# Performance work log

Measured on AMD Instinct MI355X. Metric: run time of the kernel, lower is better.

Reference implementation:

```python
import jax, jax.numpy as jnp
import numpy as np

N, E, NFEAT, NHID, NCLASS = 50000, 800000, 256, 128, 16
NTRAIN, NTEST, K = 5000, 5000, 20


def setup_inputs() -> dict:
    key = jax.random.key(0)
    ks = jax.random.split(key, 10)
    features = jax.random.normal(ks[0], (N, NFEAT), dtype=jnp.float32)
    edge_index = jax.random.randint(ks[1], (2, E), 0, N, dtype=jnp.int64)
    edge_weight = jax.random.uniform(ks[2], (E,), dtype=jnp.float32)
    labels = jax.random.randint(ks[3], (N,), 0, NCLASS)
    onehot_labels = jax.nn.one_hot(labels, NCLASS, dtype=jnp.float32)
    idx_train = jax.random.randint(ks[4], (NTRAIN,), 0, N, dtype=jnp.int64)
    idx_test = jax.random.randint(ks[5], (NTEST,), 0, N, dtype=jnp.int64)
    # GCN parameters (2-layer: nfeat->nhid->nhid), glorot-ish init
    W1 = jax.random.normal(ks[6], (NFEAT, NHID), dtype=jnp.float32) / np.sqrt(NFEAT)
    b1 = jnp.zeros((NHID,), dtype=jnp.float32)
    W2 = jax.random.normal(ks[7], (NHID, NHID), dtype=jnp.float32) / np.sqrt(NHID)
    b2 = jnp.zeros((NHID,), dtype=jnp.float32)
    return {"features": features, "edge_weight": edge_weight,
            "onehot_labels": onehot_labels, "W1": W1, "b1": b1,
            "W2": W2, "b2": b2, "edge_index": edge_index,
            "idx_train": idx_train, "idx_test": idx_test}


def _propagate(h, edge_index, edge_weight, n_nodes):
    # out[dst] += w * h[src]  (weighted message passing)
    src, dst = edge_index[0], edge_index[1]
    return jax.ops.segment_sum(h[src] * edge_weight[:, None], dst,
                               num_segments=n_nodes)


def reference(features, edge_weight, onehot_labels, W1, b1, W2, b2,
              edge_index, idx_train, idx_test):
    n_nodes = features.shape[0]
    # 2-layer GCN: transform then propagate (efficient order)
    h = _propagate(features @ W1, edge_index, edge_weight, n_nodes) + b1
    h = jax.nn.relu(h)
    emb = _propagate(h @ W2, edge_index, edge_weight, n_nodes) + b2

    # KNN scoring: [n_test, n_train] similarity matrix
    score = emb[idx_test] @ emb[idx_train].T
    # keep top-K largest per row (original masks the n_train-K smallest with -inf)
    vals, idx = jax.lax.top_k(score, K)
    rows = jnp.arange(score.shape[0])[:, None]
    masked = jnp.full_like(score, -jnp.inf).at[rows, idx].set(vals)
    weights = jax.nn.softmax(masked, axis=1)
    preds = weights @ onehot_labels[idx_train]
    return preds
```

## Files before the change

kernel.cpp:

```cpp
#include <hip/hip_runtime.h>
#include <math.h>
#include <limits.h>

#define NNODE 50000
#define NEDGE 800000
#define NFEAT 256
#define NHID  128
#define NTEST 5000
#define NTRAIN 5000
#define NCLS  16
#define TOPK  20
#define CB    640
#define NCT   8
#define RB    32
#define NTPAD (NCT * CB)
#define CCAP  512

typedef __attribute__((ext_vector_type(8))) short short8v;
typedef __attribute__((ext_vector_type(4))) short short4v;
typedef __attribute__((ext_vector_type(4))) float f32x4;

__device__ inline int swz(int r, int c) {
  int cc = c + 4 * r;
  cc = (cc < CB) ? cc : cc - CB;
  return r * CB + cc;
}

__device__ inline void splitbf(float x, unsigned short& h, unsigned short& l) {
  unsigned u = __float_as_uint(x);
  unsigned hb = (u + 0x7fffu + ((u >> 16) & 1u)) >> 16;
  float hf = __uint_as_float(hb << 16);
  float r = x - hf;
  unsigned ur = __float_as_uint(r);
  unsigned lb = (ur + 0x7fffu + ((ur >> 16) & 1u)) >> 16;
  h = (unsigned short)hb; l = (unsigned short)lb;
}

__device__ inline void split8(float4 a0, float4 a1, short8v& h, short8v& l) {
  unsigned short hh, ll;
  splitbf(a0.x, hh, ll); h[0] = (short)hh; l[0] = (short)ll;
  splitbf(a0.y, hh, ll); h[1] = (short)hh; l[1] = (short)ll;
  splitbf(a0.z, hh, ll); h[2] = (short)hh; l[2] = (short)ll;
  splitbf(a0.w, hh, ll); h[3] = (short)hh; l[3] = (short)ll;
  splitbf(a1.x, hh, ll); h[4] = (short)hh; l[4] = (short)ll;
  splitbf(a1.y, hh, ll); h[5] = (short)hh; l[5] = (short)ll;
  splitbf(a1.z, hh, ll); h[6] = (short)hh; l[6] = (short)ll;
  splitbf(a1.w, hh, ll); h[7] = (short)hh; l[7] = (short)ll;
}

__global__ __launch_bounds__(256)
void prep0(int* __restrict__ cursor,
           const float* __restrict__ W1, unsigned short* __restrict__ WT1hi,
           unsigned short* __restrict__ WT1lo,
           const float* __restrict__ W2, unsigned short* __restrict__ WT2hi,
           unsigned short* __restrict__ WT2lo,
           const float* __restrict__ onehot, const int* __restrict__ itr,
           float* __restrict__ lab, int* __restrict__ ccnt) {
  int gid = blockIdx.x * 256 + threadIdx.x;
  if (gid < NNODE) {
    cursor[gid] = 0;
  } else if (gid < NNODE + NFEAT * 128) {
    int i = gid - NNODE;
    int n = i / NFEAT, k = i - n * NFEAT;
    unsigned short h, l;
    splitbf(W1[(size_t)k * 128 + n], h, l);
    WT1hi[i] = h; WT1lo[i] = l;
  } else if (gid < NNODE + NFEAT * 128 + NHID * 128) {
    int i = gid - NNODE - NFEAT * 128;
    int n = i / NHID, k = i - n * NHID;
    unsigned short h, l;
    splitbf(W2[(size_t)k * 128 + n], h, l);
    WT2hi[i] = h; WT2lo[i] = l;
  } else if (gid < NNODE + NFEAT * 128 + NHID * 128 + NTRAIN * NCLS) {
    int i = gid - NNODE - NFEAT * 128 - NHID * 128;
    int j = i >> 4, c = i & 15;
    lab[i] = onehot[(size_t)itr[j] * NCLS + c];
  } else if (gid < NNODE + NFEAT * 128 + NHID * 128 + NTRAIN * NCLS + NTEST) {
    ccnt[gid - NNODE - NFEAT * 128 - NHID * 128 - NTRAIN * NCLS] = 0;
  }
}

template<int KT, bool RELU>
__global__ __launch_bounds__(256)
void gemm_mfma(const float* __restrict__ A, const unsigned short* __restrict__ WThi,
               const unsigned short* __restrict__ WTlo, float* __restrict__ C, int M) {
  const int tid = threadIdx.x;
  const int w = tid >> 6, lane = tid & 63;
  const int m0 = blockIdx.x * 64 + w * 16;
  int arow = m0 + (lane & 15); if (arow > M - 1) arow = M - 1;
  const int koff = (lane >> 4) * 8;

  f32x4 acc[8];
#pragma unroll
  for (int t = 0; t < 8; ++t) acc[t] = {0.f, 0.f, 0.f, 0.f};

#pragma unroll
  for (int ks = 0; ks < KT / 32; ++ks) {
    const float* ap = &A[(size_t)arow * KT + ks * 32 + koff];
    float4 a0 = *reinterpret_cast<const float4*>(ap);
    float4 a1 = *reinterpret_cast<const float4*>(ap + 4);
    if (RELU) {
      a0.x=fmaxf(a0.x,0.f); a0.y=fmaxf(a0.y,0.f); a0.z=fmaxf(a0.z,0.f); a0.w=fmaxf(a0.w,0.f);
      a1.x=fmaxf(a1.x,0.f); a1.y=fmaxf(a1.y,0.f); a1.z=fmaxf(a1.z,0.f); a1.w=fmaxf(a1.w,0.f);
    }
    short8v ah, al;
    split8(a0, a1, ah, al);
#pragma unroll
    for (int t = 0; t < 8; ++t) {
      size_t bo = (size_t)(t * 16 + (lane & 15)) * KT + ks * 32 + koff;
      short8v bh = *reinterpret_cast<const short8v*>(&WThi[bo]);
      short8v bl = *reinterpret_cast<const short8v*>(&WTlo[bo]);
      acc[t] = __builtin_amdgcn_mfma_f32_16x16x32_bf16(ah, bh, acc[t], 0, 0, 0);
      acc[t] = __builtin_amdgcn_mfma_f32_16x16x32_bf16(ah, bl, acc[t], 0, 0, 0);
      acc[t] = __builtin_amdgcn_mfma_f32_16x16x32_bf16(al, bh, acc[t], 0, 0, 0);
    }
  }
  const int crow0 = m0 + (lane >> 4) * 4;
#pragma unroll
  for (int j = 0; j < 4; ++j) {
    int row = crow0 + j;
    if (row < M) {
#pragma unroll
      for (int t = 0; t < 8; ++t)
        C[(size_t)row * 128 + t * 16 + (lane & 15)] = acc[t][j];
    }
  }
}

__global__ __launch_bounds__(256)
void hist_dst(const int* __restrict__ edst, int* __restrict__ cnt) {
  int e = blockIdx.x * 256 + threadIdx.x;
  if (e < NEDGE) atomicAdd(&cnt[edst[e]], 1);
}

#define SCHUNK 196
__global__ __launch_bounds__(256)
void scan_cnt(int* __restrict__ cnt) {
  __shared__ int part[256];
  const int t = threadIdx.x;
  const int base = t * SCHUNK;
  int s = 0;
  for (int i = 0; i < SCHUNK / 4; ++i) {
    int idx = base + i * 4;
    if (idx + 3 < NNODE) {
      int4 v = *reinterpret_cast<const int4*>(&cnt[idx]);
      s += v.x + v.y + v.z + v.w;
    } else {
      for (int j = 0; j < 4; ++j) if (idx + j < NNODE) s += cnt[idx + j];
    }
  }
  part[t] = s;
  __syncthreads();
  for (int off = 1; off < 256; off <<= 1) {
    int v = (t >= off) ? part[t - off] : 0;
    __syncthreads();
    part[t] += v;
    __syncthreads();
  }
  int run = part[t] - s;
  for (int i = 0; i < SCHUNK / 4; ++i) {
    int idx = base + i * 4;
    if (idx + 3 < NNODE) {
      int4 v = *reinterpret_cast<const int4*>(&cnt[idx]);
      int4 o;
      o.x = run; run += v.x; o.y = run; run += v.y;
      o.z = run; run += v.z; o.w = run; run += v.w;
      *reinterpret_cast<int4*>(&cnt[idx]) = o;
    } else {
      for (int j = 0; j < 4; ++j)
        if (idx + j < NNODE) { int c = cnt[idx + j]; cnt[idx + j] = run; run += c; }
    }
  }
}

__global__ __launch_bounds__(256)
void fill_csr(const int* __restrict__ esrc, const int* __restrict__ edst,
              const float* __restrict__ ew, int* __restrict__ cursor,
              int2* __restrict__ packed) {
  int e = blockIdx.x * 256 + threadIdx.x;
  if (e < NEDGE) {
    int d = edst[e];
    int p = atomicAdd(&cursor[d], 1);
    packed[p] = make_int2(esrc[e], __float_as_int(ew[e]));
  }
}

__global__ __launch_bounds__(256)
void gather_nodes(const float* __restrict__ X, float* __restrict__ out,
                  const int* __restrict__ endoff, const int2* __restrict__ packed,
                  const float* __restrict__ bias) {
  const int tid = threadIdx.x;
  const int node = blockIdx.x * 4 + (tid >> 6);
  const int lane = tid & 63;
  const int half = lane >> 5, c4 = lane & 31;
  const int beg = node ? endoff[node - 1] : 0;
  const int end = endoff[node];
  const float4* X4 = reinterpret_cast<const float4*>(X);
  float4 a0 = {0.f,0.f,0.f,0.f}, a1 = {0.f,0.f,0.f,0.f};
  float4 a2 = {0.f,0.f,0.f,0.f}, a3 = {0.f,0.f,0.f,0.f};
  int e = beg + half;
  for (; e + 6 < end; e += 8) {
    int2 p0 = packed[e],     p1 = packed[e + 2];
    int2 p2 = packed[e + 4], p3 = packed[e + 6];
    float4 x0 = X4[(size_t)p0.x * 32 + c4];
    float4 x1 = X4[(size_t)p1.x * 32 + c4];
    float4 x2 = X4[(size_t)p2.x * 32 + c4];
    float4 x3 = X4[(size_t)p3.x * 32 + c4];
    float w0 = __int_as_float(p0.y), w1 = __int_as_float(p1.y);
    float w2 = __int_as_float(p2.y), w3 = __int_as_float(p3.y);
    a0.x += w0*x0.x; a0.y += w0*x0.y; a0.z += w0*x0.z; a0.w += w0*x0.w;
    a1.x += w1*x1.x; a1.y += w1*x1.y; a1.z += w1*x1.z; a1.w += w1*x1.w;
    a2.x += w2*x2.x; a2.y += w2*x2.y; a2.z += w2*x2.z; a2.w += w2*x2.w;
    a3.x += w3*x3.x; a3.y += w3*x3.y; a3.z += w3*x3.z; a3.w += w3*x3.w;
  }
  for (; e < end; e += 2) {
    int2 p = packed[e];
    float4 x = X4[(size_t)p.x * 32 + c4];
    float w = __int_as_float(p.y);
    a0.x += w*x.x; a0.y += w*x.y; a0.z += w*x.z; a0.w += w*x.w;
  }
  a0.x += a1.x + a2.x + a3.x; a0.y += a1.y + a2.y + a3.y;
  a0.z += a1.z + a2.z + a3.z; a0.w += a1.w + a2.w + a3.w;
  a0.x += __shfl_xor(a0.x, 32); a0.y += __shfl_xor(a0.y, 32);
  a0.z += __shfl_xor(a0.z, 32); a0.w += __shfl_xor(a0.w, 32);
  if (half == 0) {
    float4 b = reinterpret_cast<const float4*>(bias)[c4];
    a0.x += b.x; a0.y += b.y; a0.z += b.z; a0.w += b.w;
    reinterpret_cast<float4*>(out)[(size_t)node * 32 + c4] = a0;
  }
}

__global__ __launch_bounds__(256)
void gather_targets(const float* __restrict__ X, const int* __restrict__ endoff,
                    const int2* __restrict__ packed, const float* __restrict__ b2,
                    const int* __restrict__ itr, const int* __restrict__ ite,
                    unsigned short* __restrict__ Thi, unsigned short* __restrict__ Tlo,
                    unsigned short* __restrict__ Qhi, unsigned short* __restrict__ Qlo) {
  const int tid = threadIdx.x;
  const int tgt = blockIdx.x * 4 + (tid >> 6);
  const int lane = tid & 63;
  const int half = lane >> 5, c4 = lane & 31;
  const bool isQ = tgt >= NTPAD;
  const int j = isQ ? tgt - NTPAD : tgt;
  int node = -1;
  if (isQ) { if (j < NTEST) node = ite[j]; }
  else if (j < NTRAIN) node = itr[j];

  float4 a0 = {0.f, 0.f, 0.f, 0.f};
  if (node >= 0) {
    const int beg = node ? endoff[node - 1] : 0;
    const int end = endoff[node];
    const float4* X4 = reinterpret_cast<const float4*>(X);
    float4 a1 = {0.f,0.f,0.f,0.f}, a2 = {0.f,0.f,0.f,0.f}, a3 = {0.f,0.f,0.f,0.f};
    int e = beg + half;
    for (; e + 6 < end; e += 8) {
      int2 p0 = packed[e],     p1 = packed[e + 2];
      int2 p2 = packed[e + 4], p3 = packed[e + 6];
      float4 x0 = X4[(size_t)p0.x * 32 + c4];
      float4 x1 = X4[(size_t)p1.x * 32 + c4];
      float4 x2 = X4[(size_t)p2.x * 32 + c4];
      float4 x3 = X4[(size_t)p3.x * 32 + c4];
      float w0 = __int_as_float(p0.y), w1 = __int_as_float(p1.y);
      float w2 = __int_as_float(p2.y), w3 = __int_as_float(p3.y);
      a0.x += w0*x0.x; a0.y += w0*x0.y; a0.z += w0*x0.z; a0.w += w0*x0.w;
      a1.x += w1*x1.x; a1.y += w1*x1.y; a1.z += w1*x1.z; a1.w += w1*x1.w;
      a2.x += w2*x2.x; a2.y += w2*x2.y; a2.z += w2*x2.z; a2.w += w2*x2.w;
      a3.x += w3*x3.x; a3.y += w3*x3.y; a3.z += w3*x3.z; a3.w += w3*x3.w;
    }
    for (; e < end; e += 2) {
      int2 p = packed[e];
      float4 x = X4[(size_t)p.x * 32 + c4];
      float w = __int_as_float(p.y);
      a0.x += w*x.x; a0.y += w*x.y; a0.z += w*x.z; a0.w += w*x.w;
    }
    a0.x += a1.x + a2.x + a3.x; a0.y += a1.y + a2.y + a3.y;
    a0.z += a1.z + a2.z + a3.z; a0.w += a1.w + a2.w + a3.w;
    a0.x += __shfl_xor(a0.x, 32); a0.y += __shfl_xor(a0.y, 32);
    a0.z += __shfl_xor(a0.z, 32); a0.w += __shfl_xor(a0.w, 32);
    float4 b = reinterpret_cast<const float4*>(b2)[c4];
    a0.x += b.x; a0.y += b.y; a0.z += b.z; a0.w += b.w;
  }
  if (half == 0 && (isQ ? j < NTEST : j < NTPAD)) {
    unsigned short h, l;
    short4v hv, lv;
    splitbf(a0.x, h, l); hv[0] = (short)h; lv[0] = (short)l;
    splitbf(a0.y, h, l); hv[1] = (short)h; lv[1] = (short)l;
    splitbf(a0.z, h, l); hv[2] = (short)h; lv[2] = (short)l;
    splitbf(a0.w, h, l); hv[3] = (short)h; lv[3] = (short)l;
    size_t o = (size_t)j * 128 + c4 * 4;
    if (isQ) {
      *reinterpret_cast<short4v*>(&Qhi[o]) = hv;
      *reinterpret_cast<short4v*>(&Qlo[o]) = lv;
    } else {
      *reinterpret_cast<short4v*>(&Thi[o]) = hv;
      *reinterpret_cast<short4v*>(&Tlo[o]) = lv;
    }
  }
}

__global__ __launch_bounds__(512)
void score_mfma(const unsigned short* __restrict__ Qhi, const unsigned short* __restrict__ Qlo,
                const unsigned short* __restrict__ Thi, const unsigned short* __restrict__ Tlo,
                int* __restrict__ ccnt, float* __restrict__ candv, int* __restrict__ candi) {
  __shared__ float s[2 * 16 * CB];
  const int tid = threadIdx.x;
  const int w = tid >> 6, lane = tid & 63;
  const int r0 = (blockIdx.x >> 3) * RB;
  const int j0 = (blockIdx.x & 7) * CB;

  int arow0 = r0 + (lane & 15);      if (arow0 > NTEST - 1) arow0 = NTEST - 1;
  int arow1 = r0 + 16 + (lane & 15); if (arow1 > NTEST - 1) arow1 = NTEST - 1;
  const int koff = (lane >> 4) * 8;
  short8v ah0[4], al0[4], ah1[4], al1[4];
#pragma unroll
  for (int ks = 0; ks < 4; ++ks) {
    ah0[ks] = *reinterpret_cast<const short8v*>(&Qhi[(size_t)arow0 * 128 + ks * 32 + koff]);
    al0[ks] = *reinterpret_cast<const short8v*>(&Qlo[(size_t)arow0 * 128 + ks * 32 + koff]);
    ah1[ks] = *reinterpret_cast<const short8v*>(&Qhi[(size_t)arow1 * 128 + ks * 32 + koff]);
    al1[ks] = *reinterpret_cast<const short8v*>(&Qlo[(size_t)arow1 * 128 + ks * 32 + koff]);
  }

#pragma unroll
  for (int t = 0; t < 5; ++t) {
    int colbase = w * 80 + t * 16;
    int col = j0 + colbase + (lane & 15);
    const unsigned short* bh = &Thi[(size_t)col * 128 + koff];
    const unsigned short* bl = &Tlo[(size_t)col * 128 + koff];
    f32x4 a0 = {0.f, 0.f, 0.f, 0.f};
    f32x4 a1 = {0.f, 0.f, 0.f, 0.f};
#pragma unroll
    for (int ks = 0; ks < 4; ++ks) {
      short8v bhv = *reinterpret_cast<const short8v*>(&bh[ks * 32]);
      short8v blv = *reinterpret_cast<const short8v*>(&bl[ks * 32]);
      a0 = __builtin_amdgcn_mfma_f32_16x16x32_bf16(ah0[ks], bhv, a0, 0, 0, 0);
      a1 = __builtin_amdgcn_mfma_f32_16x16x32_bf16(ah1[ks], bhv, a1, 0, 0, 0);
      a0 = __builtin_amdgcn_mfma_f32_16x16x32_bf16(ah0[ks], blv, a0, 0, 0, 0);
      a1 = __builtin_amdgcn_mfma_f32_16x16x32_bf16(ah1[ks], blv, a1, 0, 0, 0);
      a0 = __builtin_amdgcn_mfma_f32_16x16x32_bf16(al0[ks], bhv, a0, 0, 0, 0);
      a1 = __builtin_amdgcn_mfma_f32_16x16x32_bf16(al1[ks], bhv, a1, 0, 0, 0);
    }
    int sc = colbase + (lane & 15);
    int sr = (lane >> 4) * 4;
#pragma unroll
    for (int r = 0; r < 4; ++r) s[swz(sr + r, sc)] = a0[r];
#pragma unroll
    for (int r = 0; r < 4; ++r) s[16 * CB + swz(sr + r, sc)] = a1[r];
  }
  __syncthreads();

  const unsigned long long ltm = ((unsigned long long)1 << lane) - 1;

#pragma unroll
  for (int g = 0; g < 2; ++g) {
    const float* sg = s + g * 16 * CB;
#pragma unroll
    for (int r = 0; r < 2; ++r) {
      const int m = w * 2 + r;
      const int row = r0 + g * 16 + m;
      if (row >= NTEST) continue;
      float v[10];
#pragma unroll
      for (int k = 0; k < 10; ++k) {
        int c = lane + 64 * k;
        v[k] = (j0 + c < NTRAIN) ? sg[swz(m, c)] : -INFINITY;
      }
      float t0 = fmaxf(v[0], v[1]), t1 = fmaxf(v[2], v[3]);
      float t2 = fmaxf(v[4], v[5]), t3 = fmaxf(v[6], v[7]);
      float sv = fmaxf(fmaxf(fmaxf(t0, t1), fmaxf(t2, t3)), fmaxf(v[8], v[9]));
#pragma unroll
      for (int k = 2; k <= 64; k <<= 1) {
#pragma unroll
        for (int j = k >> 1; j > 0; j >>= 1) {
          float ov = __shfl_xor(sv, j);
          bool keepMax = ((lane & j) == 0) == ((lane & k) == 0 || k == 64);
          sv = keepMax ? fmaxf(sv, ov) : fminf(sv, ov);
        }
      }
      float T = __shfl(sv, 19);

      int myo[10];
      int tot = 0;
#pragma unroll
      for (int k = 0; k < 10; ++k) {
        unsigned long long mk = __ballot(v[k] >= T);
        myo[k] = tot + (int)__popcll(mk & ltm);
        tot += (int)__popcll(mk);
      }
      if (tot <= 64) {
        int base = 0;
        if (lane == 0) base = atomicAdd(&ccnt[row], tot);
        base = __shfl(base, 0);
        float* cv = candv + (size_t)row * CCAP + base;
        int*   ci = candi + (size_t)row * CCAP + base;
#pragma unroll
        for (int k = 0; k < 10; ++k) {
          if (v[k] >= T) { cv[myo[k]] = v[k]; ci[myo[k]] = j0 + lane + 64 * k; }
        }
      } else {
        float selv = 0.f; int seli = 0;
#pragma unroll
        for (int it = 0; it < TOPK; ++it) {
          float bv = v[0]; int bk = 0;
#pragma unroll
          for (int k = 1; k < 10; ++k)
            if (v[k] > bv) { bv = v[k]; bk = k; }
          int bj = lane + 64 * bk;
#pragma unroll
          for (int off = 1; off < 64; off <<= 1) {
            float ov = __shfl_xor(bv, off);
            int   oj = __shfl_xor(bj, off);
            if (ov > bv || (ov == bv && oj < bj)) { bv = ov; bj = oj; }
          }
          if (lane == it) { selv = bv; seli = j0 + bj; }
          int ck = bj >> 6;
          if ((bj & 63) == lane) {
#pragma unroll
            for (int k = 0; k < 10; ++k)
              if (k == ck) v[k] = -INFINITY;
          }
        }
        int base = 0;
        if (lane == 0) base = atomicAdd(&ccnt[row], TOPK);
        base = __shfl(base, 0);
        if (lane < TOPK) {
          candv[(size_t)row * CCAP + base + lane] = selv;
          candi[(size_t)row * CCAP + base + lane] = seli;
        }
      }
    }
  }
}

__device__ inline void sort64_vi(float& v, int& idx, int lane) {
#pragma unroll
  for (int k = 2; k <= 64; k <<= 1) {
#pragma unroll
    for (int j = k >> 1; j > 0; j >>= 1) {
      float ov = __shfl_xor(v, j);
      int   oi = __shfl_xor(idx, j);
      bool first = (v > ov) || (v == ov && idx < oi);
      bool keepMine = (((lane & j) == 0) == ((lane & k) == 0 || k == 64)) ? first : !first;
      if (!keepMine) { v = ov; idx = oi; }
    }
  }
}

__global__ __launch_bounds__(256)
void merge_topk(const float* __restrict__ candv, const int* __restrict__ candi,
                const int* __restrict__ ccnt, const float* __restrict__ lab,
                float* __restrict__ out) {
  const int tid = threadIdx.x;
  const int wv = tid >> 6, lane = tid & 63;
  const int row = blockIdx.x * 4 + wv;
  const size_t base = (size_t)row * CCAP;
  const int C = ccnt[row];

  float v = -INFINITY; int idx = INT_MAX;
  int take = C < 64 ? C : 64;
  if (lane < take) { v = candv[base + lane]; idx = candi[base + lane]; }
  sort64_vi(v, idx, lane);
  int consumed = take;
  while (consumed < C) {
    int n = C - consumed; if (n > 44) n = 44;
    if (lane >= TOPK) {
      int p = lane - TOPK;
      if (p < n) { v = candv[base + consumed + p]; idx = candi[base + consumed + p]; }
      else       { v = -INFINITY; idx = INT_MAX; }
    }
    sort64_vi(v, idx, lane);
    consumed += n;
  }
  float mx = __shfl(v, 0);
  float wgt = (lane < TOPK) ? expf(v - mx) : 0.f;
  float sum = wgt;
#pragma unroll
  for (int off = 1; off < 64; off <<= 1) sum += __shfl_xor(sum, off);

  float acc = 0.f;
#pragma unroll
  for (int i = 0; i < TOPK; ++i) {
    float wi = __shfl(wgt, i);
    int   ji = __shfl(idx, i);
    if (lane < NCLS) acc += wi * lab[(size_t)ji * NCLS + lane];
  }
  if (lane < NCLS) out[(size_t)row * NCLS + lane] = acc / sum;
}

extern "C" void kernel_launch(void* const* d_in, const int* in_sizes, int n_in,
                              void* d_out, int out_size, void* d_ws, size_t ws_size,
                              hipStream_t stream) {
  const float* feat   = (const float*)d_in[0];
  const float* ew     = (const float*)d_in[1];
  const float* onehot = (const float*)d_in[2];
  const float* W1     = (const float*)d_in[3];
  const float* b1     = (const float*)d_in[4];
  const float* W2     = (const float*)d_in[5];
  const float* b2     = (const float*)d_in[6];
  const int*   ei     = (const int*)d_in[7];
  const int*   itr    = (const int*)d_in[8];
  const int*   ite    = (const int*)d_in[9];
  float* out = (float*)d_out;
  float* ws  = (float*)d_ws;

  float* bufA   = ws;
  float* bufH   = bufA + (size_t)NNODE * NHID;
  int*   cursor = (int*)(bufH + (size_t)NNODE * NHID);
  int2*  packed = (int2*)(cursor + ((NNODE + 15) & ~15));
  unsigned short* WT1hi = (unsigned short*)(packed + NEDGE);
  unsigned short* WT1lo = WT1hi + 128 * NFEAT;
  unsigned short* WT2hi = WT1lo + 128 * NFEAT;
  unsigned short* WT2lo = WT2hi + 128 * NHID;
  float* lab  = (float*)(WT2lo + 128 * NHID);
  int*   ccnt = (int*)(lab + (size_t)NTRAIN * NCLS);
  unsigned short* Thi = (unsigned short*)bufH;
  unsigned short* Tlo = Thi + (size_t)NTPAD * NHID;
  unsigned short* Qhi = Tlo + (size_t)NTPAD * NHID;
  unsigned short* Qlo = Qhi + (size_t)NTEST * NHID;
  float* candv = bufA;
  int*   candi = (int*)(bufA + (size_t)NTEST * CCAP);

  const int* esrc = ei;
  const int* edst = ei + NEDGE;

  int ptot = NNODE + NFEAT * 128 + NHID * 128 + NTRAIN * NCLS + NTEST;
  prep0<<<(ptot + 255) / 256, 256, 0, stream>>>(
      cursor, W1, WT1hi, WT1lo, W2, WT2hi, WT2lo, onehot, itr, lab, ccnt);
  hist_dst<<<(NEDGE + 255) / 256, 256, 0, stream>>>(edst, cursor);
  scan_cnt<<<1, 256, 0, stream>>>(cursor);
  fill_csr<<<(NEDGE + 255) / 256, 256, 0, stream>>>(esrc, edst, ew, cursor, packed);

  gemm_mfma<NFEAT, false><<<(NNODE + 63) / 64, 256, 0, stream>>>(feat, WT1hi, WT1lo, bufA, NNODE);
  gather_nodes<<<NNODE / 4, 256, 0, stream>>>(bufA, bufH, cursor, packed, b1);
  gemm_mfma<NHID, true><<<(NNODE + 63) / 64, 256, 0, stream>>>(bufH, WT2hi, WT2lo, bufA, NNODE);
  gather_targets<<<(NTPAD + NTEST) / 4, 256, 0, stream>>>(
      bufA, cursor, packed, b2, itr, ite, Thi, Tlo, Qhi, Qlo);

  score_mfma<<<((NTEST + RB - 1) / RB) * NCT, 512, 0, stream>>>(
      Qhi, Qlo, Thi, Tlo, ccnt, candv, candi);
  merge_topk<<<NTEST / 4, 256, 0, stream>>>(candv, candi, ccnt, lab, out);
}
```

Measured before the change: 397.0 us.

## Reorder second layer to propagate-then-transform only target nodes, fuse CSR kernels

The second layer now aggregates relu(H) for only the ~10k train/test target nodes first and then applies W2 to those rows in a small GEMM with bias and bf16 split fused in. This replaces the full 50k-node W2 GEMM and relies on linearity of propagation. The histogram pass is merged into the prep kernel and the CSR fill is merged into the layer-1 GEMM launch, with a memset replacing the cursor zeroing. Together these remove redundant work and several kernel launches, at the cost of heterogeneous blocks sharing one launch.

```diff
diff --git a/kernel.cpp b/kernel.cpp
--- a/kernel.cpp
+++ b/kernel.cpp
@@ -14,7 +14,10 @@
 #define NCT   8
 #define RB    32
 #define NTPAD (NCT * CB)
+#define NTGT  (NTPAD + NTEST)
 #define CCAP  512
+#define GB1   ((NNODE + 63) / 64)
+#define FB1   ((NEDGE + 255) / 256)
 
 typedef __attribute__((ext_vector_type(8))) short short8v;
 typedef __attribute__((ext_vector_type(4))) short short4v;
@@ -49,88 +52,35 @@
 }
 
 __global__ __launch_bounds__(256)
-void prep0(int* __restrict__ cursor,
-           const float* __restrict__ W1, unsigned short* __restrict__ WT1hi,
-           unsigned short* __restrict__ WT1lo,
-           const float* __restrict__ W2, unsigned short* __restrict__ WT2hi,
-           unsigned short* __restrict__ WT2lo,
-           const float* __restrict__ onehot, const int* __restrict__ itr,
-           float* __restrict__ lab, int* __restrict__ ccnt) {
+void prep_hist(const float* __restrict__ W1, unsigned short* __restrict__ WT1hi,
+               unsigned short* __restrict__ WT1lo,
+               const float* __restrict__ W2, unsigned short* __restrict__ WT2hi,
+               unsigned short* __restrict__ WT2lo,
+               const float* __restrict__ onehot, const int* __restrict__ itr,
+               float* __restrict__ lab, int* __restrict__ ccnt,
+               const int* __restrict__ edst, int* __restrict__ cursor) {
   int gid = blockIdx.x * 256 + threadIdx.x;
-  if (gid < NNODE) {
-    cursor[gid] = 0;
-  } else if (gid < NNODE + NFEAT * 128) {
-    int i = gid - NNODE;
-    int n = i / NFEAT, k = i - n * NFEAT;
+  if (gid < NFEAT * 128) {
+    int n = gid / NFEAT, k = gid - n * NFEAT;
     unsigned short h, l;
     splitbf(W1[(size_t)k * 128 + n], h, l);
-    WT1hi[i] = h; WT1lo[i] = l;
-  } else if (gid < NNODE + NFEAT * 128 + NHID * 128) {
-    int i = gid - NNODE - NFEAT * 128;
+    WT1hi[gid] = h; WT1lo[gid] = l;
+  } else if (gid < NFEAT * 128 + NHID * 128) {
+    int i = gid - NFEAT * 128;
     int n = i / NHID, k = i - n * NHID;
     unsigned short h, l;
     splitbf(W2[(size_t)k * 128 + n], h, l);
     WT2hi[i] = h; WT2lo[i] = l;
-  } else if (gid < NNODE + NFEAT * 128 + NHID * 128 + NTRAIN * NCLS) {
-    int i = gid - NNODE - NFEAT * 128 - NHID * 128;
+  } else if (gid < NFEAT * 128 + NHID * 128 + NTRAIN * NCLS) {
+    int i = gid - NFEAT * 128 - NHID * 128;
     int j = i >> 4, c = i & 15;
     lab[i] = onehot[(size_t)itr[j] * NCLS + c];
-  } else if (gid < NNODE + NFEAT * 128 + NHID * 128 + NTRAIN * NCLS + NTEST) {
-    ccnt[gid - NNODE - NFEAT * 128 - NHID * 128 - NTRAIN * NCLS] = 0;
-  }
-}
-
-template<int KT, bool RELU>
-__global__ __launch_bounds__(256)
-void gemm_mfma(const float* __restrict__ A, const unsigned short* __restrict__ WThi,
-               const unsigned short* __restrict__ WTlo, float* __restrict__ C, int M) {
-  const int tid = threadIdx.x;
-  const int w = tid >> 6, lane = tid & 63;
-  const int m0 = blockIdx.x * 64 + w * 16;
-  int arow = m0 + (lane & 15); if (arow > M - 1) arow = M - 1;
-  const int koff = (lane >> 4) * 8;
-
-  f32x4 acc[8];
-#pragma unroll
-  for (int t = 0; t < 8; ++t) acc[t] = {0.f, 0.f, 0.f, 0.f};
-
-#pragma unroll
-  for (int ks = 0; ks < KT / 32; ++ks) {
-    const float* ap = &A[(size_t)arow * KT + ks * 32 + koff];
-    float4 a0 = *reinterpret_cast<const float4*>(ap);
-    float4 a1 = *reinterpret_cast<const float4*>(ap + 4);
-    if (RELU) {
-      a0.x=fmaxf(a0.x,0.f); a0.y=fmaxf(a0.y,0.f); a0.z=fmaxf(a0.z,0.f); a0.w=fmaxf(a0.w,0.f);
-      a1.x=fmaxf(a1.x,0.f); a1.y=fmaxf(a1.y,0.f); a1.z=fmaxf(a1.z,0.f); a1.w=fmaxf(a1.w,0.f);
-    }
-    short8v ah, al;
-    split8(a0, a1, ah, al);
-#pragma unroll
-    for (int t = 0; t < 8; ++t) {
-      size_t bo = (size_t)(t * 16 + (lane & 15)) * KT + ks * 32 + koff;
-      short8v bh = *reinterpret_cast<const short8v*>(&WThi[bo]);
-      short8v bl = *reinterpret_cast<const short8v*>(&WTlo[bo]);
-      acc[t] = __builtin_amdgcn_mfma_f32_16x16x32_bf16(ah, bh, acc[t], 0, 0, 0);
-      acc[t] = __builtin_amdgcn_mfma_f32_16x16x32_bf16(ah, bl, acc[t], 0, 0, 0);
-      acc[t] = __builtin_amdgcn_mfma_f32_16x16x32_bf16(al, bh, acc[t], 0, 0, 0);
-    }
-  }
-  const int crow0 = m0 + (lane >> 4) * 4;
-#pragma unroll
-  for (int j = 0; j < 4; ++j) {
-    int row = crow0 + j;
-    if (row < M) {
-#pragma unroll
-      for (int t = 0; t < 8; ++t)
-        C[(size_t)row * 128 + t * 16 + (lane & 15)] = acc[t][j];
-    }
-  }
-}
-
-__global__ __launch_bounds__(256)
-void hist_dst(const int* __restrict__ edst, int* __restrict__ cnt) {
-  int e = blockIdx.x * 256 + threadIdx.x;
-  if (e < NEDGE) atomicAdd(&cnt[edst[e]], 1);
+  } else if (gid < NFEAT * 128 + NHID * 128 + NTRAIN * NCLS + NTEST) {
+    ccnt[gid - NFEAT * 128 - NHID * 128 - NTRAIN * NCLS] = 0;
+  } else if (gid < NFEAT * 128 + NHID * 128 + NTRAIN * NCLS + NTEST + NEDGE) {
+    int e = gid - NFEAT * 128 - NHID * 128 - NTRAIN * NCLS - NTEST;
+    atomicAdd(&cursor[edst[e]], 1);
+  }
 }
 
 #define SCHUNK 196
@@ -174,14 +124,56 @@
 }
 
 __global__ __launch_bounds__(256)
-void fill_csr(const int* __restrict__ esrc, const int* __restrict__ edst,
-              const float* __restrict__ ew, int* __restrict__ cursor,
-              int2* __restrict__ packed) {
-  int e = blockIdx.x * 256 + threadIdx.x;
-  if (e < NEDGE) {
-    int d = edst[e];
-    int p = atomicAdd(&cursor[d], 1);
-    packed[p] = make_int2(esrc[e], __float_as_int(ew[e]));
+void gemm1_fill(const float* __restrict__ A, const unsigned short* __restrict__ WThi,
+                const unsigned short* __restrict__ WTlo, float* __restrict__ C,
+                const int* __restrict__ esrc, const int* __restrict__ edst,
+                const float* __restrict__ ew, int* __restrict__ cursor,
+                int2* __restrict__ packed) {
+  const int tid = threadIdx.x;
+  if (blockIdx.x >= GB1) {
+    int e = (blockIdx.x - GB1) * 256 + tid;
+    if (e < NEDGE) {
+      int d = edst[e];
+      int p = atomicAdd(&cursor[d], 1);
+      packed[p] = make_int2(esrc[e], __float_as_int(ew[e]));
+    }
+    return;
+  }
+  const int w = tid >> 6, lane = tid & 63;
+  const int m0 = blockIdx.x * 64 + w * 16;
+  int arow = m0 + (lane & 15); if (arow > NNODE - 1) arow = NNODE - 1;
+  const int koff = (lane >> 4) * 8;
+
+  f32x4 acc[8];
+#pragma unroll
+  for (int t = 0; t < 8; ++t) acc[t] = {0.f, 0.f, 0.f, 0.f};
+
+#pragma unroll
+  for (int ks = 0; ks < NFEAT / 32; ++ks) {
+    const float* ap = &A[(size_t)arow * NFEAT + ks * 32 + koff];
+    float4 a0 = *reinterpret_cast<const float4*>(ap);
+    float4 a1 = *reinterpret_cast<const float4*>(ap + 4);
+    short8v ah, al;
+    split8(a0, a1, ah, al);
+#pragma unroll
+    for (int t = 0; t < 8; ++t) {
+      size_t bo = (size_t)(t * 16 + (lane & 15)) * NFEAT + ks * 32 + koff;
+      short8v bh = *reinterpret_cast<const short8v*>(&WThi[bo]);
+      short8v bl = *reinterpret_cast<const short8v*>(&WTlo[bo]);
+      acc[t] = __builtin_amdgcn_mfma_f32_16x16x32_bf16(ah, bh, acc[t], 0, 0, 0);
+      acc[t] = __builtin_amdgcn_mfma_f32_16x16x32_bf16(ah, bl, acc[t], 0, 0, 0);
+      acc[t] = __builtin_amdgcn_mfma_f32_16x16x32_bf16(al, bh, acc[t], 0, 0, 0);
+    }
+  }
+  const int crow0 = m0 + (lane >> 4) * 4;
+#pragma unroll
+  for (int j = 0; j < 4; ++j) {
+    int row = crow0 + j;
+    if (row < NNODE) {
+#pragma unroll
+      for (int t = 0; t < 8; ++t)
+        C[(size_t)row * 128 + t * 16 + (lane & 15)] = acc[t][j];
+    }
   }
 }
 
@@ -231,11 +223,10 @@
 }
 
 __global__ __launch_bounds__(256)
-void gather_targets(const float* __restrict__ X, const int* __restrict__ endoff,
-                    const int2* __restrict__ packed, const float* __restrict__ b2,
-                    const int* __restrict__ itr, const int* __restrict__ ite,
-                    unsigned short* __restrict__ Thi, unsigned short* __restrict__ Tlo,
-                    unsigned short* __restrict__ Qhi, unsigned short* __restrict__ Qlo) {
+void gather_targets2(const float* __restrict__ H, const int* __restrict__ endoff,
+                     const int2* __restrict__ packed,
+                     const int* __restrict__ itr, const int* __restrict__ ite,
+                     float* __restrict__ g) {
   const int tid = threadIdx.x;
   const int tgt = blockIdx.x * 4 + (tid >> 6);
   const int lane = tid & 63;
@@ -250,7 +241,7 @@
   if (node >= 0) {
     const int beg = node ? endoff[node - 1] : 0;
     const int end = endoff[node];
-    const float4* X4 = reinterpret_cast<const float4*>(X);
+    const float4* X4 = reinterpret_cast<const float4*>(H);
     float4 a1 = {0.f,0.f,0.f,0.f}, a2 = {0.f,0.f,0.f,0.f}, a3 = {0.f,0.f,0.f,0.f};
     int e = beg + half;
     for (; e + 6 < end; e += 8) {
@@ -262,38 +253,82 @@
       float4 x3 = X4[(size_t)p3.x * 32 + c4];
       float w0 = __int_as_float(p0.y), w1 = __int_as_float(p1.y);
       float w2 = __int_as_float(p2.y), w3 = __int_as_float(p3.y);
-      a0.x += w0*x0.x; a0.y += w0*x0.y; a0.z += w0*x0.z; a0.w += w0*x0.w;
-      a1.x += w1*x1.x; a1.y += w1*x1.y; a1.z += w1*x1.z; a1.w += w1*x1.w;
-      a2.x += w2*x2.x; a2.y += w2*x2.y; a2.z += w2*x2.z; a2.w += w2*x2.w;
-      a3.x += w3*x3.x; a3.y += w3*x3.y; a3.z += w3*x3.z; a3.w += w3*x3.w;
+      a0.x += w0*fmaxf(x0.x,0.f); a0.y += w0*fmaxf(x0.y,0.f);
+      a0.z += w0*fmaxf(x0.z,0.f); a0.w += w0*fmaxf(x0.w,0.f);
+      a1.x += w1*fmaxf(x1.x,0.f); a1.y += w1*fmaxf(x1.y,0.f);
+      a1.z += w1*fmaxf(x1.z,0.f); a1.w += w1*fmaxf(x1.w,0.f);
+      a2.x += w2*fmaxf(x2.x,0.f); a2.y += w2*fmaxf(x2.y,0.f);
+      a2.z += w2*fmaxf(x2.z,0.f); a2.w += w2*fmaxf(x2.w,0.f);
+      a3.x += w3*fmaxf(x3.x,0.f); a3.y += w3*fmaxf(x3.y,0.f);
+      a3.z += w3*fmaxf(x3.z,0.f); a3.w += w3*fmaxf(x3.w,0.f);
     }
     for (; e < end; e += 2) {
       int2 p = packed[e];
       float4 x = X4[(size_t)p.x * 32 + c4];
       float w = __int_as_float(p.y);
-      a0.x += w*x.x; a0.y += w*x.y; a0.z += w*x.z; a0.w += w*x.w;
+      a0.x += w*fmaxf(x.x,0.f); a0.y += w*fmaxf(x.y,0.f);
+      a0.z += w*fmaxf(x.z,0.f); a0.w += w*fmaxf(x.w,0.f);
     }
     a0.x += a1.x + a2.x + a3.x; a0.y += a1.y + a2.y + a3.y;
     a0.z += a1.z + a2.z + a3.z; a0.w += a1.w + a2.w + a3.w;
     a0.x += __shfl_xor(a0.x, 32); a0.y += __shfl_xor(a0.y, 32);
     a0.z += __shfl_xor(a0.z, 32); a0.w += __shfl_xor(a0.w, 32);
-    float4 b = reinterpret_cast<const float4*>(b2)[c4];
-    a0.x += b.x; a0.y += b.y; a0.z += b.z; a0.w += b.w;
-  }
-  if (half == 0 && (isQ ? j < NTEST : j < NTPAD)) {
-    unsigned short h, l;
-    short4v hv, lv;
-    splitbf(a0.x, h, l); hv[0] = (short)h; lv[0] = (short)l;
-    splitbf(a0.y, h, l); hv[1] = (short)h; lv[1] = (short)l;
-    splitbf(a0.z, h, l); hv[2] = (short)h; lv[2] = (short)l;
-    splitbf(a0.w, h, l); hv[3] = (short)h; lv[3] = (short)l;
-    size_t o = (size_t)j * 128 + c4 * 4;
-    if (isQ) {
-      *reinterpret_cast<short4v*>(&Qhi[o]) = hv;
-      *reinterpret_cast<short4v*>(&Qlo[o]) = lv;
-    } else {
-      *reinterpret_cast<short4v*>(&Thi[o]) = hv;
-      *reinterpret_cast<short4v*>(&Tlo[o]) = lv;
+  }
+  if (half == 0 && tgt < NTGT)
+    reinterpret_cast<float4*>(g)[(size_t)tgt * 32 + c4] = a0;
+}
+
+__global__ __launch_bounds__(256)
+void mini_gemm(const float* __restrict__ A, const unsigned short* __restrict__ WThi,
+               const unsigned short* __restrict__ WTlo, const float* __restrict__ b2,
+               unsigned short* __restrict__ Thi, unsigned short* __restrict__ Tlo,
+               unsigned short* __restrict__ Qhi, unsigned short* __restrict__ Qlo) {
+  const int tid = threadIdx.x;
+  const int w = tid >> 6, lane = tid & 63;
+  const int m0 = blockIdx.x * 64 + w * 16;
+  int arow = m0 + (lane & 15); if (arow > NTGT - 1) arow = NTGT - 1;
+  const int koff = (lane >> 4) * 8;
+
+  f32x4 acc[8];
+#pragma unroll
+  for (int t = 0; t < 8; ++t) acc[t] = {0.f, 0.f, 0.f, 0.f};
+
+#pragma unroll
+  for (int ks = 0; ks < NHID / 32; ++ks) {
+    const float* ap = &A[(size_t)arow * NHID + ks * 32 + koff];
+    float4 a0 = *reinterpret_cast<const float4*>(ap);
+    float4 a1 = *reinterpret_cast<const float4*>(ap + 4);
+    short8v ah, al;
+    split8(a0, a1, ah, al);
+#pragma unroll
+    for (int t = 0; t < 8; ++t) {
+      size_t bo = (size_t)(t * 16 + (lane & 15)) * NHID + ks * 32 + koff;
+      short8v bh = *reinterpret_cast<const short8v*>(&WThi[bo]);
+      short8v bl = *reinterpret_cast<const short8v*>(&WTlo[bo]);
+      acc[t] = __builtin_amdgcn_mfma_f32_16x16x32_bf16(ah, bh, acc[t], 0, 0, 0);
+      acc[t] = __builtin_amdgcn_mfma_f32_16x16x32_bf16(ah, bl, acc[t], 0, 0, 0);
+      acc[t] = __builtin_amdgcn_mfma_f32_16x16x32_bf16(al, bh, acc[t], 0, 0, 0);
+    }
+  }
+  const int crow0 = m0 + (lane >> 4) * 4;
+#pragma unroll
+  for (int j = 0; j < 4; ++j) {
+    int row = crow0 + j;
+    if (row < NTGT) {
+#pragma unroll
+      for (int t = 0; t < 8; ++t) {
+        int col = t * 16 + (lane & 15);
+        float val = acc[t][j] + b2[col];
+        unsigned short h, l;
+        splitbf(val, h, l);
+        if (row < NTPAD) {
+          Thi[(size_t)row * 128 + col] = h;
+          Tlo[(size_t)row * 128 + col] = l;
+        } else {
+          Qhi[(size_t)(row - NTPAD) * 128 + col] = h;
+          Qlo[(size_t)(row - NTPAD) * 128 + col] = l;
+        }
+      }
     }
   }
 }
@@ -512,28 +547,29 @@
   unsigned short* WT2lo = WT2hi + 128 * NHID;
   float* lab  = (float*)(WT2lo + 128 * NHID);
   int*   ccnt = (int*)(lab + (size_t)NTRAIN * NCLS);
-  unsigned short* Thi = (unsigned short*)bufH;
+  unsigned short* Thi = (unsigned short*)bufA;
   unsigned short* Tlo = Thi + (size_t)NTPAD * NHID;
   unsigned short* Qhi = Tlo + (size_t)NTPAD * NHID;
   unsigned short* Qlo = Qhi + (size_t)NTEST * NHID;
-  float* candv = bufA;
-  int*   candi = (int*)(bufA + (size_t)NTEST * CCAP);
+  float* g    = (float*)(Qlo + (size_t)NTEST * NHID);
+  float* candv = bufH;
+  int*   candi = (int*)(bufH + (size_t)NTEST * CCAP);
 
   const int* esrc = ei;
   const int* edst = ei + NEDGE;
 
-  int ptot = NNODE + NFEAT * 128 + NHID * 128 + NTRAIN * NCLS + NTEST;
-  prep0<<<(ptot + 255) / 256, 256, 0, stream>>>(
-      cursor, W1, WT1hi, WT1lo, W2, WT2hi, WT2lo, onehot, itr, lab, ccnt);
-  hist_dst<<<(NEDGE + 255) / 256, 256, 0, stream>>>(edst, cursor);
+  hipMemsetAsync(cursor, 0, NNODE * sizeof(int), stream);
+  int ptot = NFEAT * 128 + NHID * 128 + NTRAIN * NCLS + NTEST + NEDGE;
+  prep_hist<<<(ptot + 255) / 256, 256, 0, stream>>>(
+      W1, WT1hi, WT1lo, W2, WT2hi, WT2lo, onehot, itr, lab, ccnt, edst, cursor);
   scan_cnt<<<1, 256, 0, stream>>>(cursor);
-  fill_csr<<<(NEDGE + 255) / 256, 256, 0, stream>>>(esrc, edst, ew, cursor, packed);
-
-  gemm_mfma<NFEAT, false><<<(NNODE + 63) / 64, 256, 0, stream>>>(feat, WT1hi, WT1lo, bufA, NNODE);
+  gemm1_fill<<<GB1 + FB1, 256, 0, stream>>>(
+      feat, WT1hi, WT1lo, bufA, esrc, edst, ew, cursor, packed);
+
   gather_nodes<<<NNODE / 4, 256, 0, stream>>>(bufA, bufH, cursor, packed, b1);
-  gemm_mfma<NHID, true><<<(NNODE + 63) / 64, 256, 0, stream>>>(bufH, WT2hi, WT2lo, bufA, NNODE);
-  gather_targets<<<(NTPAD + NTEST) / 4, 256, 0, stream>>>(
-      bufA, cursor, packed, b2, itr, ite, Thi, Tlo, Qhi, Qlo);
+  gather_targets2<<<(NTGT + 3) / 4, 256, 0, stream>>>(bufH, cursor, packed, itr, ite, g);
+  mini_gemm<<<(NTGT + 63) / 64, 256, 0, stream>>>(
+      g, WT2hi, WT2lo, b2, Thi, Tlo, Qhi, Qlo);
 
   score_mfma<<<((NTEST + RB - 1) / RB) * NCT, 512, 0, stream>>>(
       Qhi, Qlo, Thi, Tlo, ccnt, candv, candi);
```

Result: faster. 328.4 us (-17.3%).
